# Optimization experiments

Measured on AMD Instinct MI355X. Metric: run time of the kernel, lower is better.

## Reference

```python
import jax, jax.numpy as jnp
import numpy as np


def setup_inputs() -> dict:
    key = jax.random.key(0)
    ks = jax.random.split(key, 6)
    B, N, d = 8, 2048, 64
    h = jax.random.normal(ks[0], (B, N, d), dtype=jnp.float32)
    adj = jax.random.randint(ks[1], (B, N, N), 0, 2, dtype=jnp.int32)
    h_root = jax.random.normal(ks[2], (B, N), dtype=jnp.float32)
    weight = jax.random.normal(ks[3], (d, d), dtype=jnp.float32) * (1.0 / np.sqrt(d))
    a1 = jax.random.normal(ks[4], (d, 1), dtype=jnp.float32) * (1.0 / np.sqrt(d))
    a2 = jax.random.normal(ks[5], (d, 1), dtype=jnp.float32) * (1.0 / np.sqrt(d))
    return {"h": h, "adj": adj, "h_root": h_root, "weight": weight, "a1": a1, "a2": a2}


def reference(h, adj, h_root, weight, a1, a2):
    h0 = h
    hw = jax.nn.relu(jnp.matmul(h, weight))          # (B,N,d)
    t1 = jnp.matmul(hw, a1)                          # (B,N,1)
    t2 = jnp.matmul(hw, a2)                          # (B,N,1)
    # e[b,i,j] = relu(t1[b,i] + t2[b,j])  (broadcast, same as repeat/view in torch)
    e = jax.nn.relu(t1 + jnp.swapaxes(t2, -1, -2))   # (B,N,N)
    # FAITHFUL to source bug: pos0 = -9e15 * zeros_like(adj) == 0, so
    # non-edges get logit 0 (not -inf) before softmax.
    e = jnp.where(adj > 0, e, jnp.zeros_like(e))
    attention = jax.nn.softmax(e, axis=-1)           # (B,N,N)
    embedding = jnp.matmul(attention, hw)            # (B,N,d)
    # assign = h_root[:,:,None] @ ones(B,1,d) -> h_root broadcast over d;
    # assign > 0  <=>  h_root > 0 since ones are positive.
    assign = h_root[:, :, None] * jnp.ones((1, 1, hw.shape[-1]), dtype=hw.dtype)
    embedding = jnp.where(assign > 0, embedding, h0)
    return embedding
```

## Files before the change

kernel.cpp:

```cpp
#include <hip/hip_runtime.h>
#include <hip/hip_bf16.h>

#define BATCH 8
#define NN    2048
#define DD    64
#define BN    (BATCH * NN)

#define NSPLIT 4
#define JSPAN  (NN / NSPLIT)
#define JCHUNK 128
#define CHUNKS (JSPAN / JCHUNK)
#define HWST   520

typedef __attribute__((ext_vector_type(8))) short bf16x8;
typedef __attribute__((ext_vector_type(4))) float f32x4;

static __device__ __forceinline__ unsigned f2bf_pk(float lo, float hi) {
  unsigned ul = __float_as_uint(lo);
  unsigned uh = __float_as_uint(hi);
  ul = (ul + 0x7fffu + ((ul >> 16) & 1u)) >> 16;
  uh = (uh + 0x7fffu + ((uh >> 16) & 1u)) & 0xffff0000u;
  return ul | uh;
}

__global__ __launch_bounds__(256) void k1_hw_t1_t2(
    const float* __restrict__ h, const float* __restrict__ W,
    const float* __restrict__ a1, const float* __restrict__ a2,
    unsigned short* __restrict__ hwT, float* __restrict__ t1, float* __restrict__ t2) {
  __shared__ float ht[64 * 36];
  __shared__ float Ws[64 * 64];
  __shared__ unsigned short bt[64 * 40];

  const int t  = threadIdx.x;
  const int r0 = blockIdx.x * 32;

#pragma unroll
  for (int r = 0; r < 4; ++r) {
    int f = t + 256 * r;
    reinterpret_cast<float4*>(Ws)[f] = reinterpret_cast<const float4*>(W)[f];
  }
#pragma unroll
  for (int r = 0; r < 2; ++r) {
    int f = t + 256 * r;
    int i = f >> 4, j4 = f & 15;
    float4 v = reinterpret_cast<const float4*>(h + (size_t)(r0 + i) * DD)[j4];
    ht[(4 * j4 + 0) * 36 + i] = v.x;
    ht[(4 * j4 + 1) * 36 + i] = v.y;
    ht[(4 * j4 + 2) * 36 + i] = v.z;
    ht[(4 * j4 + 3) * 36 + i] = v.w;
  }
  __syncthreads();

  const int trow = t >> 4, kcol = t & 15;
  float4 acc0 = make_float4(0.f, 0.f, 0.f, 0.f);
  float4 acc1 = make_float4(0.f, 0.f, 0.f, 0.f);

#pragma unroll 8
  for (int j = 0; j < 64; ++j) {
    float2 hv = *reinterpret_cast<const float2*>(&ht[j * 36 + 2 * trow]);
    float4 wv = reinterpret_cast<const float4*>(Ws)[j * 16 + kcol];
    acc0.x = fmaf(hv.x, wv.x, acc0.x); acc0.y = fmaf(hv.x, wv.y, acc0.y);
    acc0.z = fmaf(hv.x, wv.z, acc0.z); acc0.w = fmaf(hv.x, wv.w, acc0.w);
    acc1.x = fmaf(hv.y, wv.x, acc1.x); acc1.y = fmaf(hv.y, wv.y, acc1.y);
    acc1.z = fmaf(hv.y, wv.z, acc1.z); acc1.w = fmaf(hv.y, wv.w, acc1.w);
  }

  acc0.x = fmaxf(acc0.x, 0.f); acc0.y = fmaxf(acc0.y, 0.f);
  acc0.z = fmaxf(acc0.z, 0.f); acc0.w = fmaxf(acc0.w, 0.f);
  acc1.x = fmaxf(acc1.x, 0.f); acc1.y = fmaxf(acc1.y, 0.f);
  acc1.z = fmaxf(acc1.z, 0.f); acc1.w = fmaxf(acc1.w, 0.f);

  float4 a1v = reinterpret_cast<const float4*>(a1)[kcol];
  float4 a2v = reinterpret_cast<const float4*>(a2)[kcol];
  float s1_0 = acc0.x * a1v.x + acc0.y * a1v.y + acc0.z * a1v.z + acc0.w * a1v.w;
  float s1_1 = acc1.x * a1v.x + acc1.y * a1v.y + acc1.z * a1v.z + acc1.w * a1v.w;
  float s2_0 = acc0.x * a2v.x + acc0.y * a2v.y + acc0.z * a2v.z + acc0.w * a2v.w;
  float s2_1 = acc1.x * a2v.x + acc1.y * a2v.y + acc1.z * a2v.z + acc1.w * a2v.w;
#pragma unroll
  for (int m = 1; m <= 8; m <<= 1) {
    s1_0 += __shfl_xor(s1_0, m, 64);
    s1_1 += __shfl_xor(s1_1, m, 64);
    s2_0 += __shfl_xor(s2_0, m, 64);
    s2_1 += __shfl_xor(s2_1, m, 64);
  }
  {
    int row = r0 + 2 * trow;
    if (kcol == 0) {
      t1[row] = s1_0; t1[row + 1] = s1_1;
      t2[row] = s2_0; t2[row + 1] = s2_1;
    }
  }

  {
    const float* a0 = &acc0.x;
    const float* a1p = &acc1.x;
#pragma unroll
    for (int c = 0; c < 4; ++c) {
      int k = 4 * kcol + c;
      *reinterpret_cast<unsigned*>(&bt[k * 40 + 2 * trow]) = f2bf_pk(a0[c], a1p[c]);
    }
  }
  __syncthreads();
  {
    int k = t >> 2, jp = t & 3;
    int bb = r0 >> 11;
    int jb = r0 & (NN - 1);
    *reinterpret_cast<int4*>(hwT + ((size_t)bb * DD + k) * NN + jb + jp * 8) =
        *reinterpret_cast<const int4*>(&bt[k * 40 + jp * 8]);
  }
}

__global__ __launch_bounds__(256, 2) void k2_attn(
    const unsigned short* __restrict__ hwT, const int* __restrict__ adj,
    const float* __restrict__ t1, const float* __restrict__ t2,
    float* __restrict__ pacc, float* __restrict__ pden) {
  __shared__ unsigned short hws[64 * HWST];
  __shared__ float t2s[JSPAN];

  const int t     = threadIdx.x;
  const int split = blockIdx.x >> 8;
  const int rem   = blockIdx.x & 255;
  const int b     = rem >> 5;
  const int i0    = (rem & 31) * 64;
  const int w     = t >> 6;
  const int lane  = t & 63;
  const int m     = lane & 15;
  const int quad  = lane >> 4;
  const int jbase = split * JSPAN;

  const unsigned short* hwTb = hwT + (size_t)b * DD * NN + jbase;
#pragma unroll
  for (int r = 0; r < 16; ++r) {
    int idx = t + 256 * r, k = idx >> 6, jp = idx & 63;
    *reinterpret_cast<int4*>(&hws[k * HWST + jp * 8]) =
        *reinterpret_cast<const int4*>(hwTb + (size_t)k * NN + jp * 8);
  }
  if (t < JSPAN / 4)
    *reinterpret_cast<float4*>(&t2s[t * 4]) =
        *reinterpret_cast<const float4*>(t2 + b * NN + jbase + t * 4);

  const float t1v = t1[b * NN + i0 + w * 16 + m];
  const int* adjl = adj + (size_t)(b * NN + i0 + w * 16 + m) * NN + jbase + quad * 8;

  f32x4 acc[4];
#pragma unroll
  for (int g = 0; g < 4; ++g) acc[g] = (f32x4){0.f, 0.f, 0.f, 0.f};
  float den = 0.f;

  int4 adjv[8], adjn[8];
  auto load_adj = [&](int c, int4* dst) {
    const int* ap = adjl + c * JCHUNK;
#pragma unroll
    for (int ks = 0; ks < 4; ++ks) {
      dst[2 * ks]     = *reinterpret_cast<const int4*>(ap + ks * 32);
      dst[2 * ks + 1] = *reinterpret_cast<const int4*>(ap + ks * 32 + 4);
    }
  };

  load_adj(0, adjv);
  __syncthreads();

#pragma unroll
  for (int c = 0; c < CHUNKS; ++c) {
    if (c + 1 < CHUNKS) load_adj(c + 1, adjn);

#pragma unroll
    for (int ks = 0; ks < 4; ++ks) {
      const float* t2p = &t2s[c * JCHUNK + ks * 32 + quad * 8];
      float4 e0 = *reinterpret_cast<const float4*>(t2p);
      float4 e1 = *reinterpret_cast<const float4*>(t2p + 4);
      int4 A0 = adjv[2 * ks], A1 = adjv[2 * ks + 1];
      float p0 = (A0.x > 0) ? __expf(fmaxf(t1v + e0.x, 0.f)) : 1.f;
      float p1 = (A0.y > 0) ? __expf(fmaxf(t1v + e0.y, 0.f)) : 1.f;
      float p2 = (A0.z > 0) ? __expf(fmaxf(t1v + e0.z, 0.f)) : 1.f;
      float p3 = (A0.w > 0) ? __expf(fmaxf(t1v + e0.w, 0.f)) : 1.f;
      float p4 = (A1.x > 0) ? __expf(fmaxf(t1v + e1.x, 0.f)) : 1.f;
      float p5 = (A1.y > 0) ? __expf(fmaxf(t1v + e1.y, 0.f)) : 1.f;
      float p6 = (A1.z > 0) ? __expf(fmaxf(t1v + e1.z, 0.f)) : 1.f;
      float p7 = (A1.w > 0) ? __expf(fmaxf(t1v + e1.w, 0.f)) : 1.f;
      den += ((p0 + p1) + (p2 + p3)) + ((p4 + p5) + (p6 + p7));

      union { bf16x8 v; unsigned u[4]; } Af;
      Af.u[0] = f2bf_pk(p0, p1);
      Af.u[1] = f2bf_pk(p2, p3);
      Af.u[2] = f2bf_pk(p4, p5);
      Af.u[3] = f2bf_pk(p6, p7);

#pragma unroll
      for (int g = 0; g < 4; ++g) {
        bf16x8 Bf = *reinterpret_cast<const bf16x8*>(
            &hws[(g * 16 + m) * HWST + c * JCHUNK + ks * 32 + quad * 8]);
        acc[g] = __builtin_amdgcn_mfma_f32_16x16x32_bf16(Af.v, Bf, acc[g], 0, 0, 0);
      }
    }

    if (c + 1 < CHUNKS) {
#pragma unroll
      for (int r = 0; r < 8; ++r) adjv[r] = adjn[r];
    }
  }

  den += __shfl_xor(den, 16, 64);
  den += __shfl_xor(den, 32, 64);

  const size_t sbase = (size_t)split * BN + (size_t)b * NN + i0;
  if (quad == 0) pden[sbase + w * 16 + m] = den;

  __syncthreads();
  float* os = reinterpret_cast<float*>(hws);
#pragma unroll
  for (int g = 0; g < 4; ++g)
#pragma unroll
    for (int r = 0; r < 4; ++r)
      os[(w * 16 + quad * 4 + r) * 68 + g * 16 + m] = acc[g][r];
  __syncthreads();
#pragma unroll
  for (int r2 = 0; r2 < 4; ++r2) {
    int idx = t + 256 * r2, row = idx >> 4, c4 = idx & 15;
    *reinterpret_cast<float4*>(&pacc[(sbase + row) * DD + c4 * 4]) =
        *reinterpret_cast<const float4*>(&os[row * 68 + c4 * 4]);
  }
}

__global__ __launch_bounds__(256) void k3_reduce(
    const float* __restrict__ pacc, const float* __restrict__ pden,
    const float* __restrict__ h, const float* __restrict__ h_root,
    float* __restrict__ out) {
  const int g   = blockIdx.x * 256 + threadIdx.x;
  const int row = g >> 4;
  const int k4  = g & 15;

  float4 a = make_float4(0.f, 0.f, 0.f, 0.f);
  float den = 0.f;
#pragma unroll
  for (int s = 0; s < NSPLIT; ++s) {
    const size_t prow = (size_t)s * BN + row;
    float4 p = reinterpret_cast<const float4*>(pacc + prow * DD)[k4];
    a.x += p.x; a.y += p.y; a.z += p.z; a.w += p.w;
    den += pden[prow];
  }
  const float hr = h_root[row];
  float4 res;
  if (hr > 0.f) {
    const float inv = 1.f / den;
    res.x = a.x * inv; res.y = a.y * inv; res.z = a.z * inv; res.w = a.w * inv;
  } else {
    res = reinterpret_cast<const float4*>(h)[g];
  }
  reinterpret_cast<float4*>(out)[g] = res;
}

extern "C" void kernel_launch(void* const* d_in, const int* in_sizes, int n_in,
                              void* d_out, int out_size, void* d_ws, size_t ws_size,
                              hipStream_t stream) {
  const float* h      = (const float*)d_in[0];
  const int*   adj    = (const int*)d_in[1];
  const float* h_root = (const float*)d_in[2];
  const float* W      = (const float*)d_in[3];
  const float* a1     = (const float*)d_in[4];
  const float* a2     = (const float*)d_in[5];
  float* out = (float*)d_out;

  unsigned short* hwT = (unsigned short*)d_ws;
  float* t1 = (float*)(hwT + (size_t)BN * DD);
  float* t2 = t1 + BN;
  float* pacc = t2 + BN;
  float* pden = pacc + (size_t)NSPLIT * BN * DD;

  k1_hw_t1_t2<<<BN / 32, 256, 0, stream>>>(h, W, a1, a2, hwT, t1, t2);
  k2_attn<<<NSPLIT * 256, 256, 0, stream>>>(hwT, adj, t1, t2, pacc, pden);
  k3_reduce<<<(BN * DD / 4) / 256, 256, 0, stream>>>(pacc, pden, h, h_root, out);
}
```

Before: 216.1 us.

## Split attention over 8 column spans with smaller LDS tile and shallower adj prefetch

Doubles the number of j-splits so each block handles 256 columns, halving the hw tile held in LDS and raising the occupancy target to 4 blocks per CU. The adjacency prefetch is reduced from a full 128-column chunk (16 int4 registers) to a single 32-column step. This aims at more waves in flight to hide the adj memory stream, at the cost of more partial results to reduce and less per-thread memory-level parallelism. The hunks not shown (block indexing and the reduction over splits) must also handle NSPLIT=8 for this to be correct.

```diff
diff --git a/kernel.cpp b/kernel.cpp
--- a/kernel.cpp
+++ b/kernel.cpp
@@ -6,11 +6,10 @@
 #define DD    64
 #define BN    (BATCH * NN)
 
-#define NSPLIT 4
+#define NSPLIT 8
 #define JSPAN  (NN / NSPLIT)
-#define JCHUNK 128
-#define CHUNKS (JSPAN / JCHUNK)
-#define HWST   520
+#define KSTEPS (JSPAN / 32)
+#define HWST   264
 
 typedef __attribute__((ext_vector_type(8))) short bf16x8;
 typedef __attribute__((ext_vector_type(4))) float f32x4;
@@ -110,7 +109,7 @@
   }
 }
 
-__global__ __launch_bounds__(256, 2) void k2_attn(
+__global__ __launch_bounds__(256, 4) void k2_attn(
     const unsigned short* __restrict__ hwT, const int* __restrict__ adj,
     const float* __restrict__ t1, const float* __restrict__ t2,
     float* __restrict__ pacc, float* __restrict__ pden) {
@@ -130,8 +129,8 @@
 
   const unsigned short* hwTb = hwT + (size_t)b * DD * NN + jbase;
 #pragma unroll
-  for (int r = 0; r < 16; ++r) {
-    int idx = t + 256 * r, k = idx >> 6, jp = idx & 63;
+  for (int r = 0; r < 8; ++r) {
+    int idx = t + 256 * r, k = idx >> 5, jp = idx & 31;
     *reinterpret_cast<int4*>(&hws[k * HWST + jp * 8]) =
         *reinterpret_cast<const int4*>(hwTb + (size_t)k * NN + jp * 8);
   }
@@ -147,57 +146,46 @@
   for (int g = 0; g < 4; ++g) acc[g] = (f32x4){0.f, 0.f, 0.f, 0.f};
   float den = 0.f;
 
-  int4 adjv[8], adjn[8];
-  auto load_adj = [&](int c, int4* dst) {
-    const int* ap = adjl + c * JCHUNK;
-#pragma unroll
-    for (int ks = 0; ks < 4; ++ks) {
-      dst[2 * ks]     = *reinterpret_cast<const int4*>(ap + ks * 32);
-      dst[2 * ks + 1] = *reinterpret_cast<const int4*>(ap + ks * 32 + 4);
-    }
-  };
-
-  load_adj(0, adjv);
-  __syncthreads();
-
-#pragma unroll
-  for (int c = 0; c < CHUNKS; ++c) {
-    if (c + 1 < CHUNKS) load_adj(c + 1, adjn);
-
-#pragma unroll
-    for (int ks = 0; ks < 4; ++ks) {
-      const float* t2p = &t2s[c * JCHUNK + ks * 32 + quad * 8];
-      float4 e0 = *reinterpret_cast<const float4*>(t2p);
-      float4 e1 = *reinterpret_cast<const float4*>(t2p + 4);
-      int4 A0 = adjv[2 * ks], A1 = adjv[2 * ks + 1];
-      float p0 = (A0.x > 0) ? __expf(fmaxf(t1v + e0.x, 0.f)) : 1.f;
-      float p1 = (A0.y > 0) ? __expf(fmaxf(t1v + e0.y, 0.f)) : 1.f;
-      float p2 = (A0.z > 0) ? __expf(fmaxf(t1v + e0.z, 0.f)) : 1.f;
-      float p3 = (A0.w > 0) ? __expf(fmaxf(t1v + e0.w, 0.f)) : 1.f;
-      float p4 = (A1.x > 0) ? __expf(fmaxf(t1v + e1.x, 0.f)) : 1.f;
-      float p5 = (A1.y > 0) ? __expf(fmaxf(t1v + e1.y, 0.f)) : 1.f;
-      float p6 = (A1.z > 0) ? __expf(fmaxf(t1v + e1.z, 0.f)) : 1.f;
-      float p7 = (A1.w > 0) ? __expf(fmaxf(t1v + e1.w, 0.f)) : 1.f;
-      den += ((p0 + p1) + (p2 + p3)) + ((p4 + p5) + (p6 + p7));
-
-      union { bf16x8 v; unsigned u[4]; } Af;
-      Af.u[0] = f2bf_pk(p0, p1);
-      Af.u[1] = f2bf_pk(p2, p3);
-      Af.u[2] = f2bf_pk(p4, p5);
-      Af.u[3] = f2bf_pk(p6, p7);
-
-#pragma unroll
-      for (int g = 0; g < 4; ++g) {
-        bf16x8 Bf = *reinterpret_cast<const bf16x8*>(
-            &hws[(g * 16 + m) * HWST + c * JCHUNK + ks * 32 + quad * 8]);
-        acc[g] = __builtin_amdgcn_mfma_f32_16x16x32_bf16(Af.v, Bf, acc[g], 0, 0, 0);
-      }
-    }
-
-    if (c + 1 < CHUNKS) {
-#pragma unroll
-      for (int r = 0; r < 8; ++r) adjv[r] = adjn[r];
-    }
+  int4 a0 = *reinterpret_cast<const int4*>(adjl);
+  int4 a1i = *reinterpret_cast<const int4*>(adjl + 4);
+  __syncthreads();
+
+#pragma unroll
+  for (int ks = 0; ks < KSTEPS; ++ks) {
+    int4 n0, n1;
+    if (ks + 1 < KSTEPS) {
+      const int* ap = adjl + (ks + 1) * 32;
+      n0 = *reinterpret_cast<const int4*>(ap);
+      n1 = *reinterpret_cast<const int4*>(ap + 4);
+    }
+
+    const float* t2p = &t2s[ks * 32 + quad * 8];
+    float4 e0 = *reinterpret_cast<const float4*>(t2p);
+    float4 e1 = *reinterpret_cast<const float4*>(t2p + 4);
+    float p0 = (a0.x > 0) ? __expf(fmaxf(t1v + e0.x, 0.f)) : 1.f;
+    float p1 = (a0.y > 0) ? __expf(fmaxf(t1v + e0.y, 0.f)) : 1.f;
+    float p2 = (a0.z > 0) ? __expf(fmaxf(t1v + e0.z, 0.f)) : 1.f;
+    float p3 = (a0.w > 0) ? __expf(fmaxf(t1v + e0.w, 0.f)) : 1.f;
+    float p4 = (a1i.x > 0) ? __expf(fmaxf(t1v + e1.x, 0.f)) : 1.f;
+    float p5 = (a1i.y > 0) ? __expf(fmaxf(t1v + e1.y, 0.f)) : 1.f;
+    float p6 = (a1i.z > 0) ? __expf(fmaxf(t1v + e1.z, 0.f)) : 1.f;
+    float p7 = (a1i.w > 0) ? __expf(fmaxf(t1v + e1.w, 0.f)) : 1.f;
+    den += ((p0 + p1) + (p2 + p3)) + ((p4 + p5) + (p6 + p7));
+
+    union { bf16x8 v; unsigned u[4]; } Af;
+    Af.u[0] = f2bf_pk(p0, p1);
+    Af.u[1] = f2bf_pk(p2, p3);
+    Af.u[2] = f2bf_pk(p4, p5);
+    Af.u[3] = f2bf_pk(p6, p7);
+
+#pragma unroll
+    for (int g = 0; g < 4; ++g) {
+      bf16x8 Bf = *reinterpret_cast<const bf16x8*>(
+          &hws[(g * 16 + m) * HWST + ks * 32 + quad * 8]);
+      acc[g] = __builtin_amdgcn_mfma_f32_16x16x32_bf16(Af.v, Bf, acc[g], 0, 0, 0);
+    }
+
+    a0 = n0; a1i = n1;
   }
 
   den += __shfl_xor(den, 16, 64);
```

Measured after the change: 224.4 us. +3.8%, slower.
